# Kernel optimization log

Measured on AMD Instinct MI355X. Metric: run time of the kernel, lower is better.

## Reference

```python
import jax, jax.numpy as jnp
import numpy as np

EPS = 1e-5

def _bn(x, g, b, m, v):
    # inference BatchNorm over last (channel) axis
    return (x - m) * (g * jax.lax.rsqrt(v + EPS)) + b

def setup_inputs() -> dict:
    key = jax.random.key(0)
    ks = jax.random.split(key, 20)
    B, C, H, W, HID = 4, 192, 56, 56, 384
    rn = lambda k, s: jax.random.normal(k, s, dtype=jnp.float32)
    ru = lambda k, s: jax.random.uniform(k, s, dtype=jnp.float32)
    return {
        "x": rn(ks[0], (B, C, H, W)),
        "fc1_w": rn(ks[1], (C, C)) * 0.05, "fc1_b": rn(ks[2], (C,)) * 0.05,
        "bn1_g": ru(ks[3], (C,)), "bn1_b": rn(ks[4], (C,)) * 0.05,
        "bn1_m": rn(ks[5], (C,)) * 0.05, "bn1_v": ru(ks[6], (C,)) + 0.5,
        "gcn_w": rn(ks[7], (HID, 2 * C)) * 0.05, "gcn_b": rn(ks[8], (HID,)) * 0.05,
        "bng_g": ru(ks[9], (HID,)), "bng_b": rn(ks[10], (HID,)) * 0.05,
        "bng_m": rn(ks[11], (HID,)) * 0.05, "bng_v": ru(ks[12], (HID,)) + 0.5,
        "fc2_w": rn(ks[13], (C, HID)) * 0.05, "fc2_b": rn(ks[14], (C,)) * 0.05,
        "bn2_g": ru(ks[15], (C,)), "bn2_b": rn(ks[16], (C,)) * 0.05,
        "bn2_m": rn(ks[17], (C,)) * 0.05, "bn2_v": ru(ks[18], (C,)) + 0.5,
    }

K = 9

def reference(x, fc1_w, fc1_b, bn1_g, bn1_b, bn1_m, bn1_v,
              gcn_w, gcn_b, bng_g, bng_b, bng_m, bng_v,
              fc2_w, fc2_b, bn2_g, bn2_b, bn2_m, bn2_v):
    B, C, H, W = x.shape
    N = H * W
    xf = x.reshape(B, C, N).transpose(0, 2, 1)          # [B, N, C] nodes
    shortcut = xf
    # fc1: conv1x1 + BN
    h = _bn(jnp.einsum('bnc,oc->bno', xf, fc1_w) + fc1_b, bn1_g, bn1_b, bn1_m, bn1_v)
    # dynamic kNN on detached features (negative squared distance, self included)
    hd = jax.lax.stop_gradient(h)
    sq = jnp.sum(hd * hd, axis=-1)                       # [B, N]
    dist = sq[:, :, None] - 2.0 * jnp.einsum('bnc,bmc->bnm', hd, hd) + sq[:, None, :]
    _, idx = jax.lax.top_k(-dist, K)                     # [B, N, K]
    # gather neighbor features
    x_j = jax.vmap(lambda f, i: f[i])(h, idx)            # [B, N, K, C]
    x_i = h[:, :, None, :]
    e = jnp.concatenate([jnp.broadcast_to(x_i, x_j.shape), x_j - x_i], axis=-1)  # [B,N,K,2C]
    m = jnp.einsum('bnkc,oc->bnko', e, gcn_w) + gcn_b    # [B, N, K, HID]
    g = jnp.max(m, axis=2)                               # edge-conv max aggregation
    g = jax.nn.gelu(_bn(g, bng_g, bng_b, bng_m, bng_v), approximate=False)
    # fc2 + residual
    out = _bn(jnp.einsum('bno,co->bnc', g, fc2_w) + fc2_b, bn2_g, bn2_b, bn2_m, bn2_v) + shortcut
    return out.transpose(0, 2, 1).reshape(B, C, H, W)
```

## Files before the change

kernel.cpp:

```cpp
#include <hip/hip_runtime.h>
#include <math.h>

#define N_PIX 3136
#define C_DIM 192
#define HID_DIM 384
#define KNN 9
#define EPS_BN 1e-5f

typedef __attribute__((ext_vector_type(4))) float f32x4;
typedef __attribute__((ext_vector_type(8))) short s16x8;
typedef unsigned short u16;

static const size_t OFF_H   = 0;
static const size_t OFF_SQ  = 2408448;
static const size_t OFF_H2  = 2420992;
static const size_t OFF_G2  = 0;
static const size_t OFF_PBF = 4829440;
static const size_t OFF_QBF = 7237888;
static const size_t OFF_WC2 = 9646336;
static const size_t OFF_W5  = 9793792;
static const size_t OFF_CST = 9867520;
static const size_t OFF_IDX = 9869056;
static const size_t OFF_PL  = 9981952;

__device__ inline u16 f2bf_rn(float x) {
    unsigned u = __float_as_uint(x);
    unsigned r = u + 0x7fffu + ((u >> 16) & 1u);
    return (u16)(r >> 16);
}
__device__ inline float bf2f(u16 v) { return __uint_as_float((unsigned)v << 16); }
__device__ inline void split2(float x, u16& hi, u16& lo) {
    hi = f2bf_rn(x);
    lo = f2bf_rn(x - bf2f(hi));
}

__global__ void k_prep(const float* __restrict__ gcn_w, const float* __restrict__ fc2_w,
                       const float* __restrict__ bn1_g, const float* __restrict__ bn1_b,
                       const float* __restrict__ bn1_m, const float* __restrict__ bn1_v,
                       const float* __restrict__ bng_g, const float* __restrict__ bng_b,
                       const float* __restrict__ bng_m, const float* __restrict__ bng_v,
                       const float* __restrict__ bn2_g, const float* __restrict__ bn2_b,
                       const float* __restrict__ bn2_m, const float* __restrict__ bn2_v,
                       u16* __restrict__ wc2, u16* __restrict__ w5, float* __restrict__ cst)
{
    int t = blockIdx.x * 256 + threadIdx.x;
    if (t < 768 * 192) {
        int o = t / 192, c = t % 192;
        float v = (o < 384) ? gcn_w[o * 384 + c] - gcn_w[o * 384 + 192 + c]
                            : gcn_w[(o - 384) * 384 + 192 + c];
        u16 hi, lo; split2(v, hi, lo);
        wc2[(size_t)o * 384 + c] = hi;
        wc2[(size_t)o * 384 + 192 + c] = lo;
    } else if (t < 768 * 192 + 192 * 384) {
        int u = t - 768 * 192;
        int c = u / 384, k = u % 384;
        u16 hi, lo; split2(fc2_w[(size_t)c * 384 + k], hi, lo);
        w5[(size_t)c * 768 + k] = hi;
        w5[(size_t)c * 768 + 384 + k] = lo;
    } else if (t < 768 * 192 + 192 * 384 + 768) {
        int u = t - 768 * 192 - 192 * 384;
        if (u < 192) {
            float s = bn1_g[u] / sqrtf(bn1_v[u] + EPS_BN);
            cst[u] = s; cst[192 + u] = bn1_b[u] - bn1_m[u] * s;
        } else if (u < 576) {
            int ch = u - 192;
            float s = bng_g[ch] / sqrtf(bng_v[ch] + EPS_BN);
            cst[384 + ch] = s; cst[768 + ch] = bng_b[ch] - bng_m[ch] * s;
        } else {
            int ch = u - 576;
            float s = bn2_g[ch] / sqrtf(bn2_v[ch] + EPS_BN);
            cst[1152 + ch] = s; cst[1344 + ch] = bn2_b[ch] - bn2_m[ch] * s;
        }
    }
}

__global__ __launch_bounds__(256) void k1_fc1_bn1(
    const float* __restrict__ x, const float* __restrict__ w,
    const float* __restrict__ bias, const float* __restrict__ cst,
    float* __restrict__ h)
{
    __shared__ float As[32][64];
    __shared__ float Bs[32][64];
    int bx = blockIdx.x;
    int o0 = blockIdx.y * 64;
    int b  = bx / 49;
    int n0 = (bx % 49) * 64;
    const float* xb = x + (size_t)b * C_DIM * N_PIX;
    int t = threadIdx.x;
    int tx = t & 15, ty = t >> 4;
    float acc[4][4] = {};
    for (int kc = 0; kc < 6; ++kc) {
        #pragma unroll
        for (int p = 0; p < 2; ++p) {
            int idx = t + p * 256;
            int kk = idx >> 4, j4 = idx & 15;
            float4 v = *reinterpret_cast<const float4*>(xb + (size_t)(kc * 32 + kk) * N_PIX + n0 + j4 * 4);
            *reinterpret_cast<float4*>(&As[kk][j4 * 4]) = v;
        }
        #pragma unroll
        for (int p = 0; p < 2; ++p) {
            int idx = t + p * 256;
            int oo = idx >> 3, c4 = idx & 7;
            float4 v = *reinterpret_cast<const float4*>(w + (size_t)(o0 + oo) * C_DIM + kc * 32 + c4 * 4);
            Bs[c4 * 4 + 0][oo] = v.x; Bs[c4 * 4 + 1][oo] = v.y;
            Bs[c4 * 4 + 2][oo] = v.z; Bs[c4 * 4 + 3][oo] = v.w;
        }
        __syncthreads();
        #pragma unroll
        for (int kk = 0; kk < 32; ++kk) {
            float4 av = *reinterpret_cast<const float4*>(&As[kk][ty * 4]);
            float4 bv = *reinterpret_cast<const float4*>(&Bs[kk][tx * 4]);
            float a[4] = {av.x, av.y, av.z, av.w};
            float bb[4] = {bv.x, bv.y, bv.z, bv.w};
            #pragma unroll
            for (int i = 0; i < 4; ++i)
                #pragma unroll
                for (int j = 0; j < 4; ++j) acc[i][j] += a[i] * bb[j];
        }
        __syncthreads();
    }
    #pragma unroll
    for (int i = 0; i < 4; ++i) {
        int n = n0 + ty * 4 + i;
        size_t r = (size_t)b * N_PIX + n;
        float vals[4];
        #pragma unroll
        for (int j = 0; j < 4; ++j) {
            int o = o0 + tx * 4 + j;
            vals[j] = (acc[i][j] + bias[o]) * cst[o] + cst[192 + o];
        }
        *reinterpret_cast<float4*>(h + r * C_DIM + o0 + tx * 4) =
            make_float4(vals[0], vals[1], vals[2], vals[3]);
    }
}

__global__ __launch_bounds__(256) void k_sq(const float* __restrict__ h, float* __restrict__ sq)
{
    int r = blockIdx.x * 256 + threadIdx.x;
    const float* hr = h + (size_t)r * C_DIM;
    float s = 0.f;
    #pragma unroll
    for (int c = 0; c < C_DIM; c += 4) {
        float4 v = *reinterpret_cast<const float4*>(hr + c);
        s += v.x * v.x + v.y * v.y + v.z * v.z + v.w * v.w;
    }
    sq[r] = s;
}

__global__ __launch_bounds__(256) void k_split(const float* __restrict__ h, u16* __restrict__ h2)
{
    int t = blockIdx.x * 256 + threadIdx.x;
    int base = t * 4;
    int r = base / C_DIM, c = base % C_DIM;
    float4 v = *reinterpret_cast<const float4*>(h + base);
    float f[4] = {v.x, v.y, v.z, v.w};
    u16* dst = h2 + (size_t)r * 384 + c;
    #pragma unroll
    for (int j = 0; j < 4; ++j) {
        u16 hi, lo; split2(f[j], hi, lo);
        dst[j] = hi; dst[192 + j] = lo;
    }
}

#define BSTR 408
__global__ __launch_bounds__(256) void k3_knn(
    const u16* __restrict__ h2, const float* __restrict__ sq,
    unsigned long long* __restrict__ pl)
{
    __shared__ u16 Bs[32 * BSTR];
    __shared__ float keyt[4][32 * 20];
    int bx = blockIdx.x;
    int b = bx / 343, rem = bx % 343;
    int strip = rem / 7, mc = rem % 7;
    int n0 = strip * 64;
    const u16* hb = h2 + (size_t)b * N_PIX * 384;
    const float* sqb = sq + (size_t)b * N_PIX;
    int t = threadIdx.x;
    int lane = t & 63, w = t >> 6;
    int col16 = lane & 15, g = lane >> 4;

    s16x8 a_hi[6], a_lo[6];
    {
        const u16* ar = hb + (size_t)(n0 + w * 16 + col16) * 384;
        #pragma unroll
        for (int ko = 0; ko < 6; ++ko) {
            a_hi[ko] = *reinterpret_cast<const s16x8*>(ar + ko * 32 + g * 8);
            a_lo[ko] = *reinterpret_cast<const s16x8*>(ar + 192 + ko * 32 + g * 8);
        }
    }

    int srow = lane >> 2, mseg = lane & 3;
    float sqn_r = sqb[n0 + w * 16 + srow];
    unsigned long long cand[KNN];
    #pragma unroll
    for (int q = 0; q < KNN; ++q) cand[q] = ~0ull;

    float* kt = keyt[w];
    int srow_stage = t & 31, half = t >> 5;

    for (int step = 0; step < 14; ++step) {
        int m0 = mc * 448 + step * 32;
        __syncthreads();
        {
            const u16* src = hb + (size_t)(m0 + srow_stage) * 384 + half * 48;
            u16* dst = Bs + srow_stage * BSTR + half * 48;
            #pragma unroll
            for (int c = 0; c < 6; ++c)
                *reinterpret_cast<s16x8*>(dst + c * 8) =
                    *reinterpret_cast<const s16x8*>(src + c * 8);
        }
        __syncthreads();

        f32x4 acc0 = {0.f, 0.f, 0.f, 0.f};
        f32x4 acc1 = {0.f, 0.f, 0.f, 0.f};
        const u16* b0 = Bs + col16 * BSTR + g * 8;
        const u16* b1 = Bs + (16 + col16) * BSTR + g * 8;
        #pragma unroll
        for (int ko = 0; ko < 6; ++ko) {
            s16x8 b0h = *reinterpret_cast<const s16x8*>(b0 + ko * 32);
            s16x8 b0l = *reinterpret_cast<const s16x8*>(b0 + 192 + ko * 32);
            s16x8 b1h = *reinterpret_cast<const s16x8*>(b1 + ko * 32);
            s16x8 b1l = *reinterpret_cast<const s16x8*>(b1 + 192 + ko * 32);
            acc0 = __builtin_amdgcn_mfma_f32_16x16x32_bf16(a_hi[ko], b0h, acc0, 0, 0, 0);
            acc0 = __builtin_amdgcn_mfma_f32_16x16x32_bf16(a_hi[ko], b0l, acc0, 0, 0, 0);
            acc0 = __builtin_amdgcn_mfma_f32_16x16x32_bf16(a_lo[ko], b0h, acc0, 0, 0, 0);
            acc1 = __builtin_amdgcn_mfma_f32_16x16x32_bf16(a_hi[ko], b1h, acc1, 0, 0, 0);
            acc1 = __builtin_amdgcn_mfma_f32_16x16x32_bf16(a_hi[ko], b1l, acc1, 0, 0, 0);
            acc1 = __builtin_amdgcn_mfma_f32_16x16x32_bf16(a_lo[ko], b1h, acc1, 0, 0, 0);
        }

        float sqm0 = sqb[m0 + col16];
        float sqm1 = sqb[m0 + 16 + col16];
        f32x4 k0, k1;
        #pragma unroll
        for (int i = 0; i < 4; ++i) {
            k0[i] = fmaf(-2.0f, acc0[i], sqm0);
            k1[i] = fmaf(-2.0f, acc1[i], sqm1);
        }
        *reinterpret_cast<f32x4*>(kt + col16 * 20 + g * 4) = k0;
        *reinterpret_cast<f32x4*>(kt + (16 + col16) * 20 + g * 4) = k1;
        asm volatile("" ::: "memory");

        #pragma unroll
        for (int j = 0; j < 8; ++j) {
            int ml = mseg * 8 + j;
            float dist = kt[ml * 20 + srow] + sqn_r;
            int m = m0 + ml;
            unsigned u = __float_as_uint(dist);
            u = (u & 0x80000000u) ? ~u : (u | 0x80000000u);
            unsigned long long key = ((unsigned long long)u << 32) | (unsigned)m;
            if (key < cand[KNN - 1]) {
                cand[KNN - 1] = key;
                #pragma unroll
                for (int q = KNN - 1; q > 0; --q) {
                    unsigned long long lo2 = cand[q - 1], hi2 = cand[q];
                    if (hi2 < lo2) { cand[q - 1] = hi2; cand[q] = lo2; }
                }
            }
        }
    }

    {
        int n = n0 + w * 16 + srow;
        size_t rowg = (size_t)b * N_PIX + n;
        for (int r = 0; r < KNN; ++r) {
            unsigned long long my = cand[0];
            unsigned long long gm = my;
            unsigned long long o1 = __shfl_xor(gm, 1); if (o1 < gm) gm = o1;
            unsigned long long o2 = __shfl_xor(gm, 2); if (o2 < gm) gm = o2;
            if (gm == my) {
                #pragma unroll
                for (int q = 0; q < KNN - 1; ++q) cand[q] = cand[q + 1];
                cand[KNN - 1] = ~0ull;
            }
            if (mseg == 0)
                pl[(rowg * 7 + mc) * KNN + r] = gm;
        }
    }
}

__global__ __launch_bounds__(256) void k3b_merge(
    const unsigned long long* __restrict__ pl, int* __restrict__ idxout)
{
    int r = blockIdx.x * 256 + threadIdx.x;
    const unsigned long long* base = pl + (size_t)r * 63;
    unsigned long long list[KNN];
    #pragma unroll
    for (int q = 0; q < KNN; ++q) list[q] = ~0ull;
    for (int c = 0; c < 63; ++c) {
        unsigned long long k = base[c];
        if (k < list[KNN - 1]) {
            list[KNN - 1] = k;
            #pragma unroll
            for (int q = KNN - 1; q > 0; --q) {
                unsigned long long lo = list[q - 1], hi = list[q];
                if (hi < lo) { list[q - 1] = hi; list[q] = lo; }
            }
        }
    }
    #pragma unroll
    for (int q = 0; q < KNN; ++q)
        idxout[(size_t)r * KNN + q] = (int)(list[q] & 0xffffffffu);
}

__global__ __launch_bounds__(256, 2) void k2_pq(
    const u16* __restrict__ h2, const u16* __restrict__ wc2,
    const float* __restrict__ gcnb, u16* __restrict__ Pbf, u16* __restrict__ Qbf)
{
    int r0 = blockIdx.x * 64;
    int o0 = blockIdx.y * 32;
    int t = threadIdx.x, lane = t & 63, w = t >> 6;
    int col16 = lane & 15, g = lane >> 4;

    s16x8 a_hi[6], a_lo[6];
    {
        const u16* ar = h2 + (size_t)(r0 + w * 16 + col16) * 384;
        #pragma unroll
        for (int ko = 0; ko < 6; ++ko) {
            a_hi[ko] = *reinterpret_cast<const s16x8*>(ar + ko * 32 + g * 8);
            a_lo[ko] = *reinterpret_cast<const s16x8*>(ar + 192 + ko * 32 + g * 8);
        }
    }
    const u16* br = wc2 + (size_t)(o0 + col16) * 384 + g * 8;
    f32x4 acc0 = {0.f, 0.f, 0.f, 0.f};
    f32x4 acc1 = {0.f, 0.f, 0.f, 0.f};
    #pragma unroll
    for (int ko = 0; ko < 6; ++ko) {
        s16x8 b0h = *reinterpret_cast<const s16x8*>(br + ko * 32);
        s16x8 b0l = *reinterpret_cast<const s16x8*>(br + 192 + ko * 32);
        s16x8 b1h = *reinterpret_cast<const s16x8*>(br + 16 * 384 + ko * 32);
        s16x8 b1l = *reinterpret_cast<const s16x8*>(br + 16 * 384 + 192 + ko * 32);
        acc0 = __builtin_amdgcn_mfma_f32_16x16x32_bf16(a_hi[ko], b0h, acc0, 0, 0, 0);
        acc0 = __builtin_amdgcn_mfma_f32_16x16x32_bf16(a_hi[ko], b0l, acc0, 0, 0, 0);
        acc0 = __builtin_amdgcn_mfma_f32_16x16x32_bf16(a_lo[ko], b0h, acc0, 0, 0, 0);
        acc1 = __builtin_amdgcn_mfma_f32_16x16x32_bf16(a_hi[ko], b1h, acc1, 0, 0, 0);
        acc1 = __builtin_amdgcn_mfma_f32_16x16x32_bf16(a_hi[ko], b1l, acc1, 0, 0, 0);
        acc1 = __builtin_amdgcn_mfma_f32_16x16x32_bf16(a_lo[ko], b1h, acc1, 0, 0, 0);
    }
    bool isP = (o0 < HID_DIM);
    #pragma unroll
    for (int oq = 0; oq < 2; ++oq) {
        int o = o0 + oq * 16 + col16;
        float bias = isP ? gcnb[o] : 0.0f;
        #pragma unroll
        for (int i = 0; i < 4; ++i) {
            size_t r = (size_t)(r0 + w * 16 + g * 4 + i);
            float v = (oq ? acc1[i] : acc0[i]) + bias;
            u16 bv = f2bf_rn(v);
            if (isP) Pbf[r * 384 + o] = bv;
            else     Qbf[r * 384 + (o - HID_DIM)] = bv;
        }
    }
}

__global__ __launch_bounds__(384) void k4_agg(
    const u16* __restrict__ Pbf, const u16* __restrict__ Qbf,
    const int* __restrict__ idx, const float* __restrict__ cst,
    u16* __restrict__ g2)
{
    int blk = blockIdx.x;
    int b = blk / N_PIX;
    size_t row = (size_t)blk;
    const int* id = idx + row * KNN;
    int o = threadIdx.x;
    const u16* Qb = Qbf + (size_t)b * N_PIX * 384;
    float v = -INFINITY;
    #pragma unroll
    for (int k = 0; k < KNN; ++k)
        v = fmaxf(v, bf2f(Qb[(size_t)id[k] * 384 + o]));
    float p = bf2f(Pbf[row * 384 + o]);
    float y = (p + v) * cst[384 + o] + cst[768 + o];
    float ge = 0.5f * y * (1.0f + erff(y * 0.70710678118654752f));
    u16 hi, lo; split2(ge, hi, lo);
    g2[row * 768 + o] = hi;
    g2[row * 768 + 384 + o] = lo;
}

__global__ __launch_bounds__(256, 2) void k5_fc2_bn2(
    const u16* __restrict__ g2, const u16* __restrict__ w5,
    const float* __restrict__ fc2b, const float* __restrict__ cst,
    const float* __restrict__ x, float* __restrict__ out)
{
    int bx = blockIdx.x;
    int c0 = blockIdx.y * 32;
    int b  = bx / 49;
    int n0 = (bx % 49) * 64;
    int r0 = bx * 64;
    int t = threadIdx.x, lane = t & 63, w = t >> 6;
    int col16 = lane & 15, g = lane >> 4;

    const u16* ar = g2 + (size_t)(r0 + w * 16 + col16) * 768;
    const u16* br = w5 + (size_t)(c0 + col16) * 768 + g * 8;
    f32x4 acc0 = {0.f, 0.f, 0.f, 0.f};
    f32x4 acc1 = {0.f, 0.f, 0.f, 0.f};
    #pragma unroll
    for (int kh = 0; kh < 2; ++kh) {
        s16x8 a_hi[6], a_lo[6];
        #pragma unroll
        for (int ko = 0; ko < 6; ++ko) {
            a_hi[ko] = *reinterpret_cast<const s16x8*>(ar + (kh * 6 + ko) * 32 + g * 8);
            a_lo[ko] = *reinterpret_cast<const s16x8*>(ar + 384 + (kh * 6 + ko) * 32 + g * 8);
        }
        #pragma unroll
        for (int ko = 0; ko < 6; ++ko) {
            int kk = (kh * 6 + ko) * 32;
            s16x8 b0h = *reinterpret_cast<const s16x8*>(br + kk);
            s16x8 b0l = *reinterpret_cast<const s16x8*>(br + 384 + kk);
            s16x8 b1h = *reinterpret_cast<const s16x8*>(br + 16 * 768 + kk);
            s16x8 b1l = *reinterpret_cast<const s16x8*>(br + 16 * 768 + 384 + kk);
            acc0 = __builtin_amdgcn_mfma_f32_16x16x32_bf16(a_hi[ko], b0h, acc0, 0, 0, 0);
            acc0 = __builtin_amdgcn_mfma_f32_16x16x32_bf16(a_hi[ko], b0l, acc0, 0, 0, 0);
            acc0 = __builtin_amdgcn_mfma_f32_16x16x32_bf16(a_lo[ko], b0h, acc0, 0, 0, 0);
            acc1 = __builtin_amdgcn_mfma_f32_16x16x32_bf16(a_hi[ko], b1h, acc1, 0, 0, 0);
            acc1 = __builtin_amdgcn_mfma_f32_16x16x32_bf16(a_hi[ko], b1l, acc1, 0, 0, 0);
            acc1 = __builtin_amdgcn_mfma_f32_16x16x32_bf16(a_lo[ko], b1h, acc1, 0, 0, 0);
        }
    }
    #pragma unroll
    for (int oq = 0; oq < 2; ++oq) {
        int c = c0 + oq * 16 + col16;
        float s2 = cst[1152 + c], sh2 = cst[1344 + c], bz = fc2b[c];
        #pragma unroll
        for (int i = 0; i < 4; ++i) {
            int n = n0 + w * 16 + g * 4 + i;
            size_t a = (size_t)b * C_DIM * N_PIX + (size_t)c * N_PIX + n;
            float v = (oq ? acc1[i] : acc0[i]) + bz;
            out[a] = v * s2 + sh2 + x[a];
        }
    }
}

extern "C" void kernel_launch(void* const* d_in, const int* in_sizes, int n_in,
                              void* d_out, int out_size, void* d_ws, size_t ws_size,
                              hipStream_t stream)
{
    const float* x      = (const float*)d_in[0];
    const float* fc1_w  = (const float*)d_in[1];
    const float* fc1_b  = (const float*)d_in[2];
    const float* bn1_g  = (const float*)d_in[3];
    const float* bn1_b  = (const float*)d_in[4];
    const float* bn1_m  = (const float*)d_in[5];
    const float* bn1_v  = (const float*)d_in[6];
    const float* gcn_w  = (const float*)d_in[7];
    const float* gcn_b  = (const float*)d_in[8];
    const float* bng_g  = (const float*)d_in[9];
    const float* bng_b  = (const float*)d_in[10];
    const float* bng_m  = (const float*)d_in[11];
    const float* bng_v  = (const float*)d_in[12];
    const float* fc2_w  = (const float*)d_in[13];
    const float* fc2_b  = (const float*)d_in[14];
    const float* bn2_g  = (const float*)d_in[15];
    const float* bn2_b  = (const float*)d_in[16];
    const float* bn2_m  = (const float*)d_in[17];
    const float* bn2_v  = (const float*)d_in[18];
    float* out = (float*)d_out;

    float* ws  = (float*)d_ws;
    float* h   = ws + OFF_H;
    float* sq  = ws + OFF_SQ;
    u16*   h2  = (u16*)(ws + OFF_H2);
    u16*   g2  = (u16*)(ws + OFF_G2);
    u16*   Pbf = (u16*)(ws + OFF_PBF);
    u16*   Qbf = (u16*)(ws + OFF_QBF);
    u16*   wc2 = (u16*)(ws + OFF_WC2);
    u16*   w5  = (u16*)(ws + OFF_W5);
    float* cst = ws + OFF_CST;
    int*   idx = (int*)(ws + OFF_IDX);
    unsigned long long* pl = (unsigned long long*)(ws + OFF_PL);

    k_prep<<<867, 256, 0, stream>>>(gcn_w, fc2_w,
                                    bn1_g, bn1_b, bn1_m, bn1_v,
                                    bng_g, bng_b, bng_m, bng_v,
                                    bn2_g, bn2_b, bn2_m, bn2_v, wc2, w5, cst);
    k1_fc1_bn1<<<dim3(196, 3), 256, 0, stream>>>(x, fc1_w, fc1_b, cst, h);
    k_sq<<<49, 256, 0, stream>>>(h, sq);
    k_split<<<2352, 256, 0, stream>>>(h, h2);
    k3_knn<<<1372, 256, 0, stream>>>(h2, sq, pl);
    k3b_merge<<<49, 256, 0, stream>>>(pl, idx);
    k2_pq<<<dim3(196, 24), 256, 0, stream>>>(h2, wc2, gcn_b, Pbf, Qbf);
    k4_agg<<<12544, 384, 0, stream>>>(Pbf, Qbf, idx, cst, g2);
    k5_fc2_bn2<<<dim3(196, 6), 256, 0, stream>>>(g2, w5, fc2_b, cst, x, out);
}
```

Baseline: 434.0 us.

## Fuse split and norm into fc1, async LDS loads in kNN, parallel merge

The fc1 epilogue now writes the bf16 hi/lo split directly and produces per-tile partial squared norms. This removes the fp32 h round trip and the separate sq and split kernels, and a small kernel sums the three partials. The kNN kernel stages B tiles with global_load_lds into an XOR-swizzled unpadded LDS layout instead of going through registers. The merge kernel splits each row across 4 lanes, exits early on the sorted per-chunk lists, and combines the lanes with shuffles. The new staging path depends on the swizzle index math being correct.

After: 404.3 us. -6.8%, faster.

```diff
diff --git a/kernel.cpp b/kernel.cpp
--- a/kernel.cpp
+++ b/kernel.cpp
@@ -11,7 +11,7 @@
 typedef __attribute__((ext_vector_type(8))) short s16x8;
 typedef unsigned short u16;
 
-static const size_t OFF_H   = 0;
+static const size_t OFF_SQP = 0;
 static const size_t OFF_SQ  = 2408448;
 static const size_t OFF_H2  = 2420992;
 static const size_t OFF_G2  = 0;
@@ -32,6 +32,11 @@
 __device__ inline void split2(float x, u16& hi, u16& lo) {
     hi = f2bf_rn(x);
     lo = f2bf_rn(x - bf2f(hi));
+}
+__device__ inline void gload16(const void* g, void* l) {
+    __builtin_amdgcn_global_load_lds(
+        (const __attribute__((address_space(1))) unsigned int*)g,
+        (__attribute__((address_space(3))) unsigned int*)l, 16, 0, 0);
 }
 
 __global__ void k_prep(const float* __restrict__ gcn_w, const float* __restrict__ fc2_w,
@@ -77,12 +82,13 @@
 __global__ __launch_bounds__(256) void k1_fc1_bn1(
     const float* __restrict__ x, const float* __restrict__ w,
     const float* __restrict__ bias, const float* __restrict__ cst,
-    float* __restrict__ h)
+    u16* __restrict__ h2, float* __restrict__ sqp)
 {
     __shared__ float As[32][64];
     __shared__ float Bs[32][64];
     int bx = blockIdx.x;
-    int o0 = blockIdx.y * 64;
+    int oy = blockIdx.y;
+    int o0 = oy * 64;
     int b  = bx / 49;
     int n0 = (bx % 49) * 64;
     const float* xb = x + (size_t)b * C_DIM * N_PIX;
@@ -123,51 +129,39 @@
     for (int i = 0; i < 4; ++i) {
         int n = n0 + ty * 4 + i;
         size_t r = (size_t)b * N_PIX + n;
-        float vals[4];
-        #pragma unroll
-        for (int j = 0; j < 4; ++j) {
-            int o = o0 + tx * 4 + j;
-            vals[j] = (acc[i][j] + bias[o]) * cst[o] + cst[192 + o];
-        }
-        *reinterpret_cast<float4*>(h + r * C_DIM + o0 + tx * 4) =
-            make_float4(vals[0], vals[1], vals[2], vals[3]);
-    }
-}
-
-__global__ __launch_bounds__(256) void k_sq(const float* __restrict__ h, float* __restrict__ sq)
+        ushort4 hi4, lo4;
+        float s = 0.0f;
+        {
+            float v0 = (acc[i][0] + bias[o0 + tx * 4 + 0]) * cst[o0 + tx * 4 + 0] + cst[192 + o0 + tx * 4 + 0];
+            float v1 = (acc[i][1] + bias[o0 + tx * 4 + 1]) * cst[o0 + tx * 4 + 1] + cst[192 + o0 + tx * 4 + 1];
+            float v2 = (acc[i][2] + bias[o0 + tx * 4 + 2]) * cst[o0 + tx * 4 + 2] + cst[192 + o0 + tx * 4 + 2];
+            float v3 = (acc[i][3] + bias[o0 + tx * 4 + 3]) * cst[o0 + tx * 4 + 3] + cst[192 + o0 + tx * 4 + 3];
+            s = v0 * v0 + v1 * v1 + v2 * v2 + v3 * v3;
+            u16 h_, l_;
+            split2(v0, h_, l_); hi4.x = h_; lo4.x = l_;
+            split2(v1, h_, l_); hi4.y = h_; lo4.y = l_;
+            split2(v2, h_, l_); hi4.z = h_; lo4.z = l_;
+            split2(v3, h_, l_); hi4.w = h_; lo4.w = l_;
+        }
+        *reinterpret_cast<ushort4*>(h2 + r * 384 + o0 + tx * 4) = hi4;
+        *reinterpret_cast<ushort4*>(h2 + r * 384 + 192 + o0 + tx * 4) = lo4;
+        #pragma unroll
+        for (int m = 1; m < 16; m <<= 1) s += __shfl_xor(s, m);
+        if (tx == 0) sqp[(size_t)oy * 12544 + r] = s;
+    }
+}
+
+__global__ __launch_bounds__(256) void k_sqf(const float* __restrict__ sqp, float* __restrict__ sq)
 {
     int r = blockIdx.x * 256 + threadIdx.x;
-    const float* hr = h + (size_t)r * C_DIM;
-    float s = 0.f;
-    #pragma unroll
-    for (int c = 0; c < C_DIM; c += 4) {
-        float4 v = *reinterpret_cast<const float4*>(hr + c);
-        s += v.x * v.x + v.y * v.y + v.z * v.z + v.w * v.w;
-    }
-    sq[r] = s;
-}
-
-__global__ __launch_bounds__(256) void k_split(const float* __restrict__ h, u16* __restrict__ h2)
-{
-    int t = blockIdx.x * 256 + threadIdx.x;
-    int base = t * 4;
-    int r = base / C_DIM, c = base % C_DIM;
-    float4 v = *reinterpret_cast<const float4*>(h + base);
-    float f[4] = {v.x, v.y, v.z, v.w};
-    u16* dst = h2 + (size_t)r * 384 + c;
-    #pragma unroll
-    for (int j = 0; j < 4; ++j) {
-        u16 hi, lo; split2(f[j], hi, lo);
-        dst[j] = hi; dst[192 + j] = lo;
-    }
-}
-
-#define BSTR 408
+    sq[r] = sqp[r] + sqp[12544 + r] + sqp[2 * 12544 + r];
+}
+
 __global__ __launch_bounds__(256) void k3_knn(
     const u16* __restrict__ h2, const float* __restrict__ sq,
     unsigned long long* __restrict__ pl)
 {
-    __shared__ u16 Bs[32 * BSTR];
+    __shared__ u16 Bs[32 * 384];
     __shared__ float keyt[4][32 * 20];
     int bx = blockIdx.x;
     int b = bx / 343, rem = bx % 343;
@@ -189,6 +183,18 @@
         }
     }
 
+    int rowoff[6];
+    {
+        int lb = lane * 16;
+        #pragma unroll
+        for (int f = 0; f < 6; ++f) {
+            int p = w * 6144 + f * 1024 + lb;
+            int row = p / 768;
+            int q = (p % 768) >> 4;
+            rowoff[f] = row * 768 + ((q ^ (row & 7)) << 4);
+        }
+    }
+
     int srow = lane >> 2, mseg = lane & 3;
     float sqn_r = sqb[n0 + w * 16 + srow];
     unsigned long long cand[KNN];
@@ -196,31 +202,31 @@
     for (int q = 0; q < KNN; ++q) cand[q] = ~0ull;
 
     float* kt = keyt[w];
-    int srow_stage = t & 31, half = t >> 5;
+    const char* hbB = (const char*)hb;
+    char* BsB = (char*)Bs;
+    int sw = (col16 & 7) << 3;
 
     for (int step = 0; step < 14; ++step) {
         int m0 = mc * 448 + step * 32;
+        size_t mbase = (size_t)m0 * 768;
         __syncthreads();
-        {
-            const u16* src = hb + (size_t)(m0 + srow_stage) * 384 + half * 48;
-            u16* dst = Bs + srow_stage * BSTR + half * 48;
-            #pragma unroll
-            for (int c = 0; c < 6; ++c)
-                *reinterpret_cast<s16x8*>(dst + c * 8) =
-                    *reinterpret_cast<const s16x8*>(src + c * 8);
-        }
+        #pragma unroll
+        for (int f = 0; f < 6; ++f)
+            gload16(hbB + mbase + rowoff[f], BsB + w * 6144 + f * 1024);
         __syncthreads();
 
         f32x4 acc0 = {0.f, 0.f, 0.f, 0.f};
         f32x4 acc1 = {0.f, 0.f, 0.f, 0.f};
-        const u16* b0 = Bs + col16 * BSTR + g * 8;
-        const u16* b1 = Bs + (16 + col16) * BSTR + g * 8;
+        const u16* brow0 = Bs + col16 * 384;
+        const u16* brow1 = Bs + (16 + col16) * 384;
         #pragma unroll
         for (int ko = 0; ko < 6; ++ko) {
-            s16x8 b0h = *reinterpret_cast<const s16x8*>(b0 + ko * 32);
-            s16x8 b0l = *reinterpret_cast<const s16x8*>(b0 + 192 + ko * 32);
-            s16x8 b1h = *reinterpret_cast<const s16x8*>(b1 + ko * 32);
-            s16x8 b1l = *reinterpret_cast<const s16x8*>(b1 + 192 + ko * 32);
+            int ch = (4 * ko + g) << 3;
+            int cl = (24 + 4 * ko + g) << 3;
+            s16x8 b0h = *reinterpret_cast<const s16x8*>(brow0 + (ch ^ sw));
+            s16x8 b0l = *reinterpret_cast<const s16x8*>(brow0 + (cl ^ sw));
+            s16x8 b1h = *reinterpret_cast<const s16x8*>(brow1 + (ch ^ sw));
+            s16x8 b1l = *reinterpret_cast<const s16x8*>(brow1 + (cl ^ sw));
             acc0 = __builtin_amdgcn_mfma_f32_16x16x32_bf16(a_hi[ko], b0h, acc0, 0, 0, 0);
             acc0 = __builtin_amdgcn_mfma_f32_16x16x32_bf16(a_hi[ko], b0l, acc0, 0, 0, 0);
             acc0 = __builtin_amdgcn_mfma_f32_16x16x32_bf16(a_lo[ko], b0h, acc0, 0, 0, 0);
@@ -282,25 +288,40 @@
 __global__ __launch_bounds__(256) void k3b_merge(
     const unsigned long long* __restrict__ pl, int* __restrict__ idxout)
 {
-    int r = blockIdx.x * 256 + threadIdx.x;
+    int t = threadIdx.x;
+    int r = blockIdx.x * 64 + (t >> 2);
+    int s = t & 3;
     const unsigned long long* base = pl + (size_t)r * 63;
-    unsigned long long list[KNN];
-    #pragma unroll
-    for (int q = 0; q < KNN; ++q) list[q] = ~0ull;
-    for (int c = 0; c < 63; ++c) {
-        unsigned long long k = base[c];
-        if (k < list[KNN - 1]) {
-            list[KNN - 1] = k;
+    unsigned long long cand[KNN];
+    #pragma unroll
+    for (int q = 0; q < KNN; ++q) cand[q] = ~0ull;
+    for (int c = s; c < 7; c += 4) {
+        const unsigned long long* ch = base + c * 9;
+        #pragma unroll
+        for (int q2 = 0; q2 < 9; ++q2) {
+            unsigned long long k = ch[q2];
+            if (k >= cand[KNN - 1]) break;
+            cand[KNN - 1] = k;
             #pragma unroll
             for (int q = KNN - 1; q > 0; --q) {
-                unsigned long long lo = list[q - 1], hi = list[q];
-                if (hi < lo) { list[q - 1] = hi; list[q] = lo; }
+                unsigned long long lo = cand[q - 1], hi = cand[q];
+                if (hi < lo) { cand[q - 1] = hi; cand[q] = lo; }
             }
         }
     }
-    #pragma unroll
-    for (int q = 0; q < KNN; ++q)
-        idxout[(size_t)r * KNN + q] = (int)(list[q] & 0xffffffffu);
+    for (int rr = 0; rr < KNN; ++rr) {
+        unsigned long long my = cand[0];
+        unsigned long long gm = my;
+        unsigned long long o1 = __shfl_xor(gm, 1); if (o1 < gm) gm = o1;
+        unsigned long long o2 = __shfl_xor(gm, 2); if (o2 < gm) gm = o2;
+        if (gm == my) {
+            #pragma unroll
+            for (int q = 0; q < KNN - 1; ++q) cand[q] = cand[q + 1];
+            cand[KNN - 1] = ~0ull;
+        }
+        if (s == 0)
+            idxout[(size_t)r * KNN + rr] = (int)(gm & 0xffffffffu);
+    }
 }
 
 __global__ __launch_bounds__(256, 2) void k2_pq(
@@ -456,7 +477,7 @@
     float* out = (float*)d_out;
 
     float* ws  = (float*)d_ws;
-    float* h   = ws + OFF_H;
+    float* sqp = ws + OFF_SQP;
     float* sq  = ws + OFF_SQ;
     u16*   h2  = (u16*)(ws + OFF_H2);
     u16*   g2  = (u16*)(ws + OFF_G2);
@@ -472,11 +493,10 @@
                                     bn1_g, bn1_b, bn1_m, bn1_v,
                                     bng_g, bng_b, bng_m, bng_v,
                                     bn2_g, bn2_b, bn2_m, bn2_v, wc2, w5, cst);
-    k1_fc1_bn1<<<dim3(196, 3), 256, 0, stream>>>(x, fc1_w, fc1_b, cst, h);
-    k_sq<<<49, 256, 0, stream>>>(h, sq);
-    k_split<<<2352, 256, 0, stream>>>(h, h2);
+    k1_fc1_bn1<<<dim3(196, 3), 256, 0, stream>>>(x, fc1_w, fc1_b, cst, h2, sqp);
+    k_sqf<<<49, 256, 0, stream>>>(sqp, sq);
     k3_knn<<<1372, 256, 0, stream>>>(h2, sq, pl);
-    k3b_merge<<<49, 256, 0, stream>>>(pl, idx);
+    k3b_merge<<<196, 256, 0, stream>>>(pl, idx);
     k2_pq<<<dim3(196, 24), 256, 0, stream>>>(h2, wc2, gcn_b, Pbf, Qbf);
     k4_agg<<<12544, 384, 0, stream>>>(Pbf, Qbf, idx, cst, g2);
     k5_fc2_bn2<<<dim3(196, 6), 256, 0, stream>>>(g2, w5, fc2_b, cst, x, out);
```
